# Performance work log

Measured on AMD Instinct MI355X. Metric: run time of the kernel, lower is better.

Reference implementation:

```python
import jax, jax.numpy as jnp
import numpy as np

B, S, D, H, DH = 4, 2048, 512, 8, 64  # batch, seq, input_dim, heads, per-head output_dim


def setup_inputs() -> dict:
    key = jax.random.key(0)
    ks = jax.random.split(key, 10)
    scale = 0.02
    inp = {
        "x": jax.random.normal(ks[0], (B, S, D), dtype=jnp.float32),
        "biological_mask": jnp.ones((B, S), dtype=bool),
        "Wq": jax.random.normal(ks[1], (D, H * DH), dtype=jnp.float32) * scale,
        "bq": jnp.zeros((H * DH,), dtype=jnp.float32),
        "Wk": jax.random.normal(ks[2], (D, H * DH), dtype=jnp.float32) * scale,
        "bk": jnp.zeros((H * DH,), dtype=jnp.float32),
        "Wv": jax.random.normal(ks[3], (D, H * DH), dtype=jnp.float32) * scale,
        "bv": jnp.zeros((H * DH,), dtype=jnp.float32),
        "Wo": jax.random.normal(ks[4], (H * DH, DH), dtype=jnp.float32) * scale,
        "bo": jnp.zeros((DH,), dtype=jnp.float32),
        "prior_weight": jnp.full((1,), 0.1, dtype=jnp.float32),
    }
    return inp


def reference(x, biological_mask, Wq, bq, Wk, bk, Wv, bv, Wo, bo, prior_weight):
    b, s, _ = x.shape
    inv_sqrt_dh = jnp.float32(1.0 / np.sqrt(DH))
    # projections -> [B,H,S,DH]
    q = (x @ Wq + bq).reshape(b, s, H, DH).transpose(0, 2, 1, 3)
    k = (x @ Wk + bk).reshape(b, s, H, DH).transpose(0, 2, 1, 3)
    v = (x @ Wv + bv).reshape(b, s, H, DH).transpose(0, 2, 1, 3)
    # scores [B,H,S,S]
    scores = jnp.einsum("bhqd,bhkd->bhqk", q, k) * inv_sqrt_dh
    # biological prior: identity matrix, broadcast over batch and heads
    prior = jnp.eye(s, dtype=scores.dtype)[None, None, :, :]
    scores = scores + prior_weight[0] * prior
    attn = jax.nn.softmax(scores, axis=-1)  # dropout is identity in eval mode
    attended = jnp.einsum("bhqk,bhkd->bhqd", attn, v)
    attended = attended.transpose(0, 2, 1, 3).reshape(b, s, H * DH)
    return attended @ Wo + bo
```

## Files before the change

### kernel.cpp

```cpp
#include <hip/hip_runtime.h>
#include <hip/hip_bf16.h>

#define B_ 4
#define S_ 2048
#define D_ 512
#define H_ 8
#define DH_ 64
#define HD_ 512
#define M_ 8192
#define QKVN 1536
#define QKN 1024
#define LOG2E 1.4426950408889634f

typedef __attribute__((ext_vector_type(8))) short bf16x8;
typedef __attribute__((ext_vector_type(4))) float f32x4;
typedef unsigned short u16;

__device__ inline u16 f2bf(float f) {
    __hip_bfloat16 h = __float2bfloat16(f);
    return *reinterpret_cast<u16*>(&h);
}

__device__ inline void async_cp16(const void* g, void* l) {
    __builtin_amdgcn_global_load_lds(
        (const __attribute__((address_space(1))) unsigned int*)g,
        (__attribute__((address_space(3))) unsigned int*)l, 16, 0, 0);
}

__global__ __launch_bounds__(256) void castbf(const float* __restrict__ src,
                                              u16* __restrict__ dst, int n8)
{
    int i = blockIdx.x * 256 + threadIdx.x;
    if (i < n8) {
        float4 a = *reinterpret_cast<const float4*>(&src[(size_t)i * 8]);
        float4 b = *reinterpret_cast<const float4*>(&src[(size_t)i * 8 + 4]);
        bf16x8 o;
        o[0] = f2bf(a.x); o[1] = f2bf(a.y); o[2] = f2bf(a.z); o[3] = f2bf(a.w);
        o[4] = f2bf(b.x); o[5] = f2bf(b.y); o[6] = f2bf(b.z); o[7] = f2bf(b.w);
        *reinterpret_cast<bf16x8*>(&dst[(size_t)i * 8]) = o;
    }
}

__global__ __launch_bounds__(256) void wprep(
    const float* __restrict__ Wq, const float* __restrict__ Wk,
    const float* __restrict__ Wv, const float* __restrict__ Wo,
    u16* __restrict__ WqkvT, u16* __restrict__ WoT)
{
    const int z = blockIdx.z;
    const float* src; u16* dst; int R, C;
    if (z < 3) { src = (z == 0) ? Wq : (z == 1) ? Wk : Wv;
                 dst = WqkvT + (size_t)z * 512 * 512; R = 512; C = 512; }
    else       { if (blockIdx.x) return; src = Wo; dst = WoT; R = 512; C = 64; }

    __shared__ u16 T[64][65];
    const int tid = threadIdx.x;
    const int c0 = blockIdx.x * 64, r0 = blockIdx.y * 64;
#pragma unroll
    for (int i = 0; i < 4; ++i) {
        int idx = i * 256 + tid;
        int r = idx >> 4, q4 = (idx & 15) << 2;
        float4 vv = *reinterpret_cast<const float4*>(&src[(size_t)(r0 + r) * C + c0 + q4]);
        T[r][q4 + 0] = f2bf(vv.x); T[r][q4 + 1] = f2bf(vv.y);
        T[r][q4 + 2] = f2bf(vv.z); T[r][q4 + 3] = f2bf(vv.w);
    }
    __syncthreads();
#pragma unroll
    for (int i = 0; i < 2; ++i) {
        int idx = i * 256 + tid;
        int cc = idx >> 3, jj = idx & 7;
        bf16x8 o;
#pragma unroll
        for (int e = 0; e < 8; ++e) o[e] = (short)T[jj * 8 + e][cc];
        *reinterpret_cast<bf16x8*>(&dst[(size_t)(c0 + cc) * R + r0 + jj * 8]) = o;
    }
}

__global__ __launch_bounds__(256) void gemm_qkv(
    const u16* __restrict__ A, const u16* __restrict__ BT,
    const float* __restrict__ bq, const float* __restrict__ bk,
    const float* __restrict__ bv, u16* __restrict__ qk,
    u16* __restrict__ vT, float qscale)
{
    __shared__ __align__(16) u16 As[128 * 64];
    __shared__ __align__(16) u16 Bs[128 * 64];
    const int tid = threadIdx.x, lane = tid & 63, w = tid >> 6;
    const int l15 = lane & 15, l4 = lane >> 4;
    const int tm = blockIdx.y * 128, tn = blockIdx.x * 128;
    const int wm = (w >> 1) * 64, wn = (w & 1) * 64;

    f32x4 acc[4][4] = {};

    for (int k0 = 0; k0 < 512; k0 += 64) {
#pragma unroll
        for (int i = 0; i < 4; ++i) {
            int call = w * 4 + i;
            int c = call * 64 + lane;
            int r = c >> 3, j = c & 7;
            async_cp16(A + (size_t)(tm + r) * 512 + k0 + ((j ^ (r & 7)) << 3),
                       &As[call * 512]);
            async_cp16(BT + (size_t)(tn + r) * 512 + k0 + ((j ^ (r & 7)) << 3),
                       &Bs[call * 512]);
        }
        __syncthreads();
#pragma unroll
        for (int ks = 0; ks < 2; ++ks) {
            bf16x8 af[4], bf[4];
#pragma unroll
            for (int mf = 0; mf < 4; ++mf) {
                int r = wm + mf * 16 + l15;
                int j = ks * 4 + l4;
                af[mf] = *reinterpret_cast<const bf16x8*>(&As[(r * 8 + (j ^ (r & 7))) * 8]);
            }
#pragma unroll
            for (int nf = 0; nf < 4; ++nf) {
                int r = wn + nf * 16 + l15;
                int j = ks * 4 + l4;
                bf[nf] = *reinterpret_cast<const bf16x8*>(&Bs[(r * 8 + (j ^ (r & 7))) * 8]);
            }
#pragma unroll
            for (int mf = 0; mf < 4; ++mf)
#pragma unroll
                for (int nf = 0; nf < 4; ++nf)
                    acc[mf][nf] = __builtin_amdgcn_mfma_f32_16x16x32_bf16(
                        af[mf], bf[nf], acc[mf][nf], 0, 0, 0);
        }
        __syncthreads();
    }
#pragma unroll
    for (int nf = 0; nf < 4; ++nf) {
        const int col = tn + wn + nf * 16 + l15;
        if (col < QKN) {
            const float bias_v = (col < 512) ? bq[col] : bk[col - 512];
            const float scl = (col < 512) ? qscale : 1.0f;
#pragma unroll
            for (int mf = 0; mf < 4; ++mf)
#pragma unroll
                for (int r = 0; r < 4; ++r) {
                    int row = tm + wm + mf * 16 + l4 * 4 + r;
                    qk[(size_t)row * QKN + col] = f2bf((acc[mf][nf][r] + bias_v) * scl);
                }
        } else {
            const int dcol = col - QKN;
            const float bias_v = bv[dcol];
            const int hh = dcol >> 6, dd = dcol & 63;
#pragma unroll
            for (int mf = 0; mf < 4; ++mf) {
                int row0 = tm + wm + mf * 16 + l4 * 4;
                int bb = row0 >> 11, s0 = row0 & 2047;
                ushort4 pk;
                pk.x = f2bf(acc[mf][nf][0] + bias_v);
                pk.y = f2bf(acc[mf][nf][1] + bias_v);
                pk.z = f2bf(acc[mf][nf][2] + bias_v);
                pk.w = f2bf(acc[mf][nf][3] + bias_v);
                *reinterpret_cast<ushort4*>(
                    &vT[((size_t)(bb * 8 + hh) * 64 + dd) * S_ + s0]) = pk;
            }
        }
    }
}

__global__ __launch_bounds__(256) void flash_mfma(
    const u16* __restrict__ qk, const u16* __restrict__ vT,
    const float* __restrict__ pw_ptr, u16* __restrict__ att)
{
    __shared__ __align__(16) u16 Kb[2][4096];
    __shared__ __align__(16) u16 Vb[2][4096];
    __shared__ __align__(16) u16 Ps[4][1024];

    const int tid = threadIdx.x, lane = tid & 63, w = tid >> 6;
    const int l15 = lane & 15, l4 = lane >> 4;
    const int bid = blockIdx.x;
    const int x = bid & 7, g = bid >> 3;
    const int bh = x * 4 + (g >> 5), qt = g & 31;
    const int h = bh & 7, b = bh >> 3;
    const float pwl = pw_ptr[0] * LOG2E;

    const u16* qbase = qk + (size_t)b * S_ * QKN + h * 64;
    const u16* kbase = qbase + 512;
    const u16* vtb   = vT + (size_t)bh * DH_ * S_;

    const int sq = qt * 64 + w * 16 + l15;
    bf16x8 qa0 = *reinterpret_cast<const bf16x8*>(&qbase[(size_t)sq * QKN + l4 * 8]);
    bf16x8 qa1 = *reinterpret_cast<const bf16x8*>(&qbase[(size_t)sq * QKN + 32 + l4 * 8]);

    f32x4 accv[4] = {};
    float l_r[4] = {};

#define STAGE(buf, jj) do {                                                        \
    _Pragma("unroll")                                                              \
    for (int i_ = 0; i_ < 2; ++i_) {                                               \
        int call_ = w * 2 + i_;                                                    \
        int c_ = call_ * 64 + lane;                                                \
        int r_ = c_ >> 3, j_ = c_ & 7;                                             \
        async_cp16(kbase + (size_t)((jj) + r_) * QKN + ((j_ ^ (r_ & 7)) << 3),     \
                   &Kb[buf][call_ * 512]);                                         \
        async_cp16(vtb + (size_t)r_ * S_ + (jj) + ((j_ ^ (r_ & 7)) << 3),          \
                   &Vb[buf][call_ * 512]);                                         \
    } } while (0)

    STAGE(0, 0);
    __syncthreads();
    int cur = 0;

    for (int t = 0; t < 32; ++t) {
        const int j0 = t << 6;
        if (t < 31) STAGE(cur ^ 1, j0 + 64);

        f32x4 s[4] = {};
        __builtin_amdgcn_s_setprio(1);
#pragma unroll
        for (int c = 0; c < 4; ++c)
#pragma unroll
            for (int ks = 0; ks < 2; ++ks) {
                int rr = c * 16 + l15;
                int j = ks * 4 + l4;
                bf16x8 kb = *reinterpret_cast<const bf16x8*>(
                    &Kb[cur][(rr * 8 + (j ^ (rr & 7))) * 8]);
                s[c] = __builtin_amdgcn_mfma_f32_16x16x32_bf16(
                    (ks == 0) ? qa0 : qa1, kb, s[c], 0, 0, 0);
            }
        __builtin_amdgcn_s_setprio(0);

        if (t == qt) {
#pragma unroll
            for (int c = 0; c < 4; ++c) {
                int col_g = j0 + c * 16 + l15;
#pragma unroll
                for (int r = 0; r < 4; ++r)
                    if (qt * 64 + w * 16 + l4 * 4 + r == col_g) s[c][r] += pwl;
            }
        }

#pragma unroll
        for (int c = 0; c < 4; ++c)
#pragma unroll
            for (int r = 0; r < 4; ++r) {
                float p = exp2f(s[c][r]);
                l_r[r] += p;
                int rr = l4 * 4 + r;
                Ps[w][rr * 64 + ((c * 16 + l15) ^ ((rr & 7) << 3))] = f2bf(p);
            }

        bf16x8 pa0 = *reinterpret_cast<const bf16x8*>(
            &Ps[w][l15 * 64 + (((0 * 4 + l4) ^ (l15 & 7)) << 3)]);
        bf16x8 pa1 = *reinterpret_cast<const bf16x8*>(
            &Ps[w][l15 * 64 + (((1 * 4 + l4) ^ (l15 & 7)) << 3)]);

        __builtin_amdgcn_s_setprio(1);
#pragma unroll
        for (int n = 0; n < 4; ++n)
#pragma unroll
            for (int ks = 0; ks < 2; ++ks) {
                int d = n * 16 + l15;
                int j = ks * 4 + l4;
                bf16x8 vb = *reinterpret_cast<const bf16x8*>(
                    &Vb[cur][(d * 8 + (j ^ (d & 7))) * 8]);
                accv[n] = __builtin_amdgcn_mfma_f32_16x16x32_bf16(
                    (ks == 0) ? pa0 : pa1, vb, accv[n], 0, 0, 0);
            }
        __builtin_amdgcn_s_setprio(0);

        __syncthreads();
        cur ^= 1;
    }
#undef STAGE

#pragma unroll
    for (int r = 0; r < 4; ++r) {
        float tsum = l_r[r];
        tsum += __shfl_xor(tsum, 1); tsum += __shfl_xor(tsum, 2);
        tsum += __shfl_xor(tsum, 4); tsum += __shfl_xor(tsum, 8);
        float inv = 1.0f / tsum;
        int row = qt * 64 + w * 16 + l4 * 4 + r;
#pragma unroll
        for (int n = 0; n < 4; ++n)
            att[(size_t)(b * S_ + row) * HD_ + h * 64 + n * 16 + l15] =
                f2bf(accv[n][r] * inv);
    }
}

__global__ __launch_bounds__(64) void out_proj(
    const u16* __restrict__ att, const u16* __restrict__ WoT,
    const float* __restrict__ bo, float* __restrict__ out)
{
    const int lane = threadIdx.x;
    const int l15 = lane & 15, l4 = lane >> 4;
    const int row0 = blockIdx.x * 16;

    f32x4 acc[4] = {};
#pragma unroll 4
    for (int ks = 0; ks < 16; ++ks) {
        bf16x8 a = *reinterpret_cast<const bf16x8*>(
            &att[(size_t)(row0 + l15) * 512 + ks * 32 + l4 * 8]);
#pragma unroll
        for (int nf = 0; nf < 4; ++nf) {
            bf16x8 bb = *reinterpret_cast<const bf16x8*>(
                &WoT[(size_t)(nf * 16 + l15) * 512 + ks * 32 + l4 * 8]);
            acc[nf] = __builtin_amdgcn_mfma_f32_16x16x32_bf16(a, bb, acc[nf], 0, 0, 0);
        }
    }
#pragma unroll
    for (int nf = 0; nf < 4; ++nf) {
        int n = nf * 16 + l15;
        float bias_v = bo[n];
#pragma unroll
        for (int r = 0; r < 4; ++r)
            out[(size_t)(row0 + l4 * 4 + r) * 64 + n] = acc[nf][r] + bias_v;
    }
}

extern "C" void kernel_launch(void* const* d_in, const int* in_sizes, int n_in,
                              void* d_out, int out_size, void* d_ws, size_t ws_size,
                              hipStream_t stream)
{
    const float* x  = (const float*)d_in[0];
    const float* Wq = (const float*)d_in[2];
    const float* bq = (const float*)d_in[3];
    const float* Wk = (const float*)d_in[4];
    const float* bk = (const float*)d_in[5];
    const float* Wv = (const float*)d_in[6];
    const float* bv = (const float*)d_in[7];
    const float* Wo = (const float*)d_in[8];
    const float* bo = (const float*)d_in[9];
    const float* pw = (const float*)d_in[10];

    u16* ws = (u16*)d_ws;
    size_t o = 0;
    u16* xb    = ws + o; o += (size_t)M_ * D_;
    u16* WqkvT = ws + o; o += (size_t)QKVN * D_;
    u16* WoT   = ws + o; o += (size_t)DH_ * HD_;
    u16* qkb   = ws + o; o += (size_t)M_ * QKN;
    u16* vTt   = ws + o; o += (size_t)M_ * HD_;
    u16* att   = ws + o; o += (size_t)M_ * HD_;

    dim3 blk(256);
    castbf<<<dim3(M_ * D_ / 8 / 256), blk, 0, stream>>>(x, xb, M_ * D_ / 8);
    wprep<<<dim3(8, 8, 4), blk, 0, stream>>>(Wq, Wk, Wv, Wo, WqkvT, WoT);

    gemm_qkv<<<dim3(QKVN / 128, M_ / 128), blk, 0, stream>>>(
        xb, WqkvT, bq, bk, bv, qkb, vTt, 0.125f * LOG2E);

    flash_mfma<<<dim3(1024), blk, 0, stream>>>(qkb, vTt, pw, att);

    out_proj<<<dim3(M_ / 16), dim3(64), 0, stream>>>(att, WoT, bo, (float*)d_out);
}
```

Baseline: 120.9 us.

## Double flash query tile per block and load V directly from global

Each block now handles 128 query rows, with each wave covering 32 rows as two 16-row fragments, so every K tile in LDS is reused across twice as many queries. The grid shrinks from 1024 to 512 blocks. The score MMA is transposed (K as A operand, Q as B), P is written to LDS with packed 64-bit stores, and V fragments are read straight from global memory rather than staged through LDS. This cuts LDS traffic and K reloads, but it raises register pressure, halves the number of blocks, and exposes uncached global V load latency inside the loop.

```diff
diff --git a/kernel.cpp b/kernel.cpp
--- a/kernel.cpp
+++ b/kernel.cpp
@@ -15,6 +15,7 @@
 typedef __attribute__((ext_vector_type(8))) short bf16x8;
 typedef __attribute__((ext_vector_type(4))) float f32x4;
 typedef unsigned short u16;
+typedef unsigned int u32;
 
 __device__ inline u16 f2bf(float f) {
     __hip_bfloat16 h = __float2bfloat16(f);
@@ -164,14 +165,13 @@
     const float* __restrict__ pw_ptr, u16* __restrict__ att)
 {
     __shared__ __align__(16) u16 Kb[2][4096];
-    __shared__ __align__(16) u16 Vb[2][4096];
-    __shared__ __align__(16) u16 Ps[4][1024];
+    __shared__ __align__(16) u16 Ps[4][2048];
 
     const int tid = threadIdx.x, lane = tid & 63, w = tid >> 6;
     const int l15 = lane & 15, l4 = lane >> 4;
     const int bid = blockIdx.x;
     const int x = bid & 7, g = bid >> 3;
-    const int bh = x * 4 + (g >> 5), qt = g & 31;
+    const int bh = x * 4 + (g >> 4), qt = g & 15;
     const int h = bh & 7, b = bh >> 3;
     const float pwl = pw_ptr[0] * LOG2E;
 
@@ -179,12 +179,18 @@
     const u16* kbase = qbase + 512;
     const u16* vtb   = vT + (size_t)bh * DH_ * S_;
 
-    const int sq = qt * 64 + w * 16 + l15;
-    bf16x8 qa0 = *reinterpret_cast<const bf16x8*>(&qbase[(size_t)sq * QKN + l4 * 8]);
-    bf16x8 qa1 = *reinterpret_cast<const bf16x8*>(&qbase[(size_t)sq * QKN + 32 + l4 * 8]);
-
-    f32x4 accv[4] = {};
-    float l_r[4] = {};
+    const int qrow0 = qt * 128 + w * 32;
+    bf16x8 qb_[2][2];
+#pragma unroll
+    for (int nf = 0; nf < 2; ++nf)
+#pragma unroll
+        for (int ks = 0; ks < 2; ++ks)
+            qb_[nf][ks] = *reinterpret_cast<const bf16x8*>(
+                &qbase[(size_t)(qrow0 + nf * 16 + l15) * QKN + ks * 32 + l4 * 8]);
+
+    f32x4 accv[2][4] = {};
+    float l_r[2] = {0.f, 0.f};
+    const int diag_t = qrow0 >> 6;
 
 #define STAGE(buf, jj) do {                                                        \
     _Pragma("unroll")                                                              \
@@ -194,69 +200,86 @@
         int r_ = c_ >> 3, j_ = c_ & 7;                                             \
         async_cp16(kbase + (size_t)((jj) + r_) * QKN + ((j_ ^ (r_ & 7)) << 3),     \
                    &Kb[buf][call_ * 512]);                                         \
-        async_cp16(vtb + (size_t)r_ * S_ + (jj) + ((j_ ^ (r_ & 7)) << 3),          \
-                   &Vb[buf][call_ * 512]);                                         \
     } } while (0)
 
     STAGE(0, 0);
     __syncthreads();
     int cur = 0;
 
-    for (int t = 0; t < 32; ++t) {
+    for (int t = 0; t < 16 * 2; ++t) {
         const int j0 = t << 6;
         if (t < 31) STAGE(cur ^ 1, j0 + 64);
 
-        f32x4 s[4] = {};
+        bf16x8 vb_[4][2];
+#pragma unroll
+        for (int nf = 0; nf < 4; ++nf)
+#pragma unroll
+            for (int ks = 0; ks < 2; ++ks)
+                vb_[nf][ks] = *reinterpret_cast<const bf16x8*>(
+                    &vtb[(size_t)(nf * 16 + l15) * S_ + j0 + ks * 32 + l4 * 8]);
+
+        f32x4 s[4][2] = {};
         __builtin_amdgcn_s_setprio(1);
 #pragma unroll
         for (int c = 0; c < 4; ++c)
 #pragma unroll
             for (int ks = 0; ks < 2; ++ks) {
                 int rr = c * 16 + l15;
-                int j = ks * 4 + l4;
-                bf16x8 kb = *reinterpret_cast<const bf16x8*>(
-                    &Kb[cur][(rr * 8 + (j ^ (rr & 7))) * 8]);
-                s[c] = __builtin_amdgcn_mfma_f32_16x16x32_bf16(
-                    (ks == 0) ? qa0 : qa1, kb, s[c], 0, 0, 0);
+                int jj2 = ks * 4 + l4;
+                bf16x8 ka = *reinterpret_cast<const bf16x8*>(
+                    &Kb[cur][(rr * 8 + (jj2 ^ (rr & 7))) * 8]);
+                s[c][0] = __builtin_amdgcn_mfma_f32_16x16x32_bf16(ka, qb_[0][ks], s[c][0], 0, 0, 0);
+                s[c][1] = __builtin_amdgcn_mfma_f32_16x16x32_bf16(ka, qb_[1][ks], s[c][1], 0, 0, 0);
             }
         __builtin_amdgcn_s_setprio(0);
 
-        if (t == qt) {
+        if (t == diag_t) {
+#pragma unroll
+            for (int c = 0; c < 4; ++c)
+#pragma unroll
+                for (int nf = 0; nf < 2; ++nf)
+#pragma unroll
+                    for (int r = 0; r < 4; ++r)
+                        if (j0 + c * 16 + l4 * 4 + r == qrow0 + nf * 16 + l15)
+                            s[c][nf][r] += pwl;
+        }
+
+#pragma unroll
+        for (int nf = 0; nf < 2; ++nf) {
+            const int prow = nf * 16 + l15;
+            const int pswz = (prow & 7) << 3;
 #pragma unroll
             for (int c = 0; c < 4; ++c) {
-                int col_g = j0 + c * 16 + l15;
-#pragma unroll
-                for (int r = 0; r < 4; ++r)
-                    if (qt * 64 + w * 16 + l4 * 4 + r == col_g) s[c][r] += pwl;
-            }
-        }
-
-#pragma unroll
-        for (int c = 0; c < 4; ++c)
-#pragma unroll
-            for (int r = 0; r < 4; ++r) {
-                float p = exp2f(s[c][r]);
-                l_r[r] += p;
-                int rr = l4 * 4 + r;
-                Ps[w][rr * 64 + ((c * 16 + l15) ^ ((rr & 7) << 3))] = f2bf(p);
-            }
-
-        bf16x8 pa0 = *reinterpret_cast<const bf16x8*>(
-            &Ps[w][l15 * 64 + (((0 * 4 + l4) ^ (l15 & 7)) << 3)]);
-        bf16x8 pa1 = *reinterpret_cast<const bf16x8*>(
-            &Ps[w][l15 * 64 + (((1 * 4 + l4) ^ (l15 & 7)) << 3)]);
+                float p0 = exp2f(s[c][nf][0]);
+                float p1 = exp2f(s[c][nf][1]);
+                float p2 = exp2f(s[c][nf][2]);
+                float p3 = exp2f(s[c][nf][3]);
+                l_r[nf] += (p0 + p1) + (p2 + p3);
+                uint2 pk;
+                pk.x = (u32)f2bf(p0) | ((u32)f2bf(p1) << 16);
+                pk.y = (u32)f2bf(p2) | ((u32)f2bf(p3) << 16);
+                *reinterpret_cast<uint2*>(
+                    &Ps[w][prow * 64 + ((c * 16 + l4 * 4) ^ pswz)]) = pk;
+            }
+        }
+
+        bf16x8 pa[2][2];
+#pragma unroll
+        for (int mf = 0; mf < 2; ++mf)
+#pragma unroll
+            for (int ks = 0; ks < 2; ++ks) {
+                int prow = mf * 16 + l15;
+                pa[mf][ks] = *reinterpret_cast<const bf16x8*>(
+                    &Ps[w][prow * 64 + ((ks * 32 + l4 * 8) ^ ((prow & 7) << 3))]);
+            }
 
         __builtin_amdgcn_s_setprio(1);
 #pragma unroll
-        for (int n = 0; n < 4; ++n)
+        for (int nf = 0; nf < 4; ++nf)
 #pragma unroll
             for (int ks = 0; ks < 2; ++ks) {
-                int d = n * 16 + l15;
-                int j = ks * 4 + l4;
-                bf16x8 vb = *reinterpret_cast<const bf16x8*>(
-                    &Vb[cur][(d * 8 + (j ^ (d & 7))) * 8]);
-                accv[n] = __builtin_amdgcn_mfma_f32_16x16x32_bf16(
-                    (ks == 0) ? pa0 : pa1, vb, accv[n], 0, 0, 0);
+                accv[0][nf] = __builtin_amdgcn_mfma_f32_16x16x32_bf16(pa[0][ks], vb_[nf][ks], accv[0][nf], 0, 0, 0);
+                accv[1][nf] = __builtin_amdgcn_mfma_f32_16x16x32_bf16(pa[1][ks], vb_[nf][ks], accv[1][nf], 0, 0, 0);
             }
         __builtin_amdgcn_s_setprio(0);
 
@@ -265,18 +288,25 @@
     }
 #undef STAGE
 
-#pragma unroll
-    for (int r = 0; r < 4; ++r) {
-        float tsum = l_r[r];
-        tsum += __shfl_xor(tsum, 1); tsum += __shfl_xor(tsum, 2);
-        tsum += __shfl_xor(tsum, 4); tsum += __shfl_xor(tsum, 8);
-        float inv = 1.0f / tsum;
-        int row = qt * 64 + w * 16 + l4 * 4 + r;
-#pragma unroll
-        for (int n = 0; n < 4; ++n)
-            att[(size_t)(b * S_ + row) * HD_ + h * 64 + n * 16 + l15] =
-                f2bf(accv[n][r] * inv);
-    }
+    float lt[2];
+#pragma unroll
+    for (int nf = 0; nf < 2; ++nf) {
+        float t2 = l_r[nf];
+        t2 += __shfl_xor(t2, 16);
+        t2 += __shfl_xor(t2, 32);
+        lt[nf] = t2;
+    }
+#pragma unroll
+    for (int mf = 0; mf < 2; ++mf)
+#pragma unroll
+        for (int r = 0; r < 4; ++r) {
+            float inv = 1.0f / __shfl(lt[mf], l4 * 4 + r);
+            int row = qrow0 + mf * 16 + l4 * 4 + r;
+#pragma unroll
+            for (int nf = 0; nf < 4; ++nf)
+                att[(size_t)(b * S_ + row) * HD_ + h * 64 + nf * 16 + l15] =
+                    f2bf(accv[mf][nf][r] * inv);
+        }
 }
 
 __global__ __launch_bounds__(64) void out_proj(
@@ -340,7 +370,7 @@
     gemm_qkv<<<dim3(QKVN / 128, M_ / 128), blk, 0, stream>>>(
         xb, WqkvT, bq, bk, bv, qkb, vTt, 0.125f * LOG2E);
 
-    flash_mfma<<<dim3(1024), blk, 0, stream>>>(qkb, vTt, pw, att);
+    flash_mfma<<<dim3(512), blk, 0, stream>>>(qkb, vTt, pw, att);
 
     out_proj<<<dim3(M_ / 16), dim3(64), 0, stream>>>(att, WoT, bo, (float*)d_out);
 }
```

Measured after the change: 129.4 us. 1.07x slower.

## Compute transposed QK^T in registers to feed PV MFMA without LDS round-trip

Applied to the files above, without the earlier changes.

Swaps MFMA operand order so the score tile comes out transposed (keys along the register dimension), and permutes K rows at staging time so each lane's score registers directly form the bf16x8 A-operand for the PV MFMA. This removes the per-wave Ps LDS buffer, its stores/loads, and the associated bank traffic. The row sum now reduces across lanes via xor 16/32 and is fetched with a shuffle at the end. Launch bounds add a min-blocks hint of 4, which may constrain registers.

```diff
diff --git a/kernel.cpp b/kernel.cpp
--- a/kernel.cpp
+++ b/kernel.cpp
@@ -159,13 +159,12 @@
     }
 }
 
-__global__ __launch_bounds__(256) void flash_mfma(
+__global__ __launch_bounds__(256, 4) void flash_mfma(
     const u16* __restrict__ qk, const u16* __restrict__ vT,
     const float* __restrict__ pw_ptr, u16* __restrict__ att)
 {
     __shared__ __align__(16) u16 Kb[2][4096];
     __shared__ __align__(16) u16 Vb[2][4096];
-    __shared__ __align__(16) u16 Ps[4][1024];
 
     const int tid = threadIdx.x, lane = tid & 63, w = tid >> 6;
     const int l15 = lane & 15, l4 = lane >> 4;
@@ -179,22 +178,28 @@
     const u16* kbase = qbase + 512;
     const u16* vtb   = vT + (size_t)bh * DH_ * S_;
 
-    const int sq = qt * 64 + w * 16 + l15;
-    bf16x8 qa0 = *reinterpret_cast<const bf16x8*>(&qbase[(size_t)sq * QKN + l4 * 8]);
-    bf16x8 qa1 = *reinterpret_cast<const bf16x8*>(&qbase[(size_t)sq * QKN + 32 + l4 * 8]);
+    const int qrow0 = qt * 64 + w * 16;
+    bf16x8 qb[2];
+#pragma unroll
+    for (int ks2 = 0; ks2 < 2; ++ks2)
+        qb[ks2] = *reinterpret_cast<const bf16x8*>(
+            &qbase[(size_t)(qrow0 + l15) * QKN + ks2 * 32 + l4 * 8]);
 
     f32x4 accv[4] = {};
-    float l_r[4] = {};
+    float l_r = 0.f;
+    const int diag_t = qt;
 
 #define STAGE(buf, jj) do {                                                        \
     _Pragma("unroll")                                                              \
     for (int i_ = 0; i_ < 2; ++i_) {                                               \
         int call_ = w * 2 + i_;                                                    \
         int c_ = call_ * 64 + lane;                                                \
-        int r_ = c_ >> 3, j_ = c_ & 7;                                             \
-        async_cp16(kbase + (size_t)((jj) + r_) * QKN + ((j_ ^ (r_ & 7)) << 3),     \
+        int rho_ = c_ >> 3, j_ = c_ & 7;                                           \
+        int pi_ = (rho_ & 32) | ((rho_ & 12) << 1) | ((rho_ & 16) >> 2)            \
+                | (rho_ & 3);                                                      \
+        async_cp16(kbase + (size_t)((jj) + pi_) * QKN + ((j_ ^ (rho_ & 7)) << 3),  \
                    &Kb[buf][call_ * 512]);                                         \
-        async_cp16(vtb + (size_t)r_ * S_ + (jj) + ((j_ ^ (r_ & 7)) << 3),          \
+        async_cp16(vtb + (size_t)rho_ * S_ + (jj) + ((j_ ^ (rho_ & 7)) << 3),      \
                    &Vb[buf][call_ * 512]);                                         \
     } } while (0)
 
@@ -211,53 +216,49 @@
 #pragma unroll
         for (int c = 0; c < 4; ++c)
 #pragma unroll
+            for (int ks2 = 0; ks2 < 2; ++ks2) {
+                const int rr = c * 16 + l15;
+                const int sl = ks2 * 4 + l4;
+                bf16x8 ka = *reinterpret_cast<const bf16x8*>(
+                    &Kb[cur][(rr * 8 + (sl ^ (rr & 7))) * 8]);
+                s[c] = __builtin_amdgcn_mfma_f32_16x16x32_bf16(ka, qb[ks2], s[c], 0, 0, 0);
+            }
+        __builtin_amdgcn_s_setprio(0);
+
+        if (t == diag_t) {
+#pragma unroll
+            for (int c = 0; c < 4; ++c)
+#pragma unroll
+                for (int r = 0; r < 4; ++r) {
+                    int kv = (c >> 1) * 32 + l4 * 8 + (c & 1) * 4 + r;
+                    if (j0 + kv == qrow0 + l15) s[c][r] += pwl;
+                }
+        }
+
+        bf16x8 pa[2];
+#pragma unroll
+        for (int ks = 0; ks < 2; ++ks)
+#pragma unroll
+            for (int d2 = 0; d2 < 2; ++d2)
+#pragma unroll
+                for (int r = 0; r < 4; ++r) {
+                    float p = exp2f(s[ks * 2 + d2][r]);
+                    l_r += p;
+                    pa[ks][d2 * 4 + r] = (short)f2bf(p);
+                }
+
+        __builtin_amdgcn_s_setprio(1);
+#pragma unroll
+        for (int nf = 0; nf < 4; ++nf) {
+            const int d = nf * 16 + l15;
+#pragma unroll
             for (int ks = 0; ks < 2; ++ks) {
-                int rr = c * 16 + l15;
-                int j = ks * 4 + l4;
-                bf16x8 kb = *reinterpret_cast<const bf16x8*>(
-                    &Kb[cur][(rr * 8 + (j ^ (rr & 7))) * 8]);
-                s[c] = __builtin_amdgcn_mfma_f32_16x16x32_bf16(
-                    (ks == 0) ? qa0 : qa1, kb, s[c], 0, 0, 0);
-            }
-        __builtin_amdgcn_s_setprio(0);
-
-        if (t == qt) {
-#pragma unroll
-            for (int c = 0; c < 4; ++c) {
-                int col_g = j0 + c * 16 + l15;
-#pragma unroll
-                for (int r = 0; r < 4; ++r)
-                    if (qt * 64 + w * 16 + l4 * 4 + r == col_g) s[c][r] += pwl;
-            }
-        }
-
-#pragma unroll
-        for (int c = 0; c < 4; ++c)
-#pragma unroll
-            for (int r = 0; r < 4; ++r) {
-                float p = exp2f(s[c][r]);
-                l_r[r] += p;
-                int rr = l4 * 4 + r;
-                Ps[w][rr * 64 + ((c * 16 + l15) ^ ((rr & 7) << 3))] = f2bf(p);
-            }
-
-        bf16x8 pa0 = *reinterpret_cast<const bf16x8*>(
-            &Ps[w][l15 * 64 + (((0 * 4 + l4) ^ (l15 & 7)) << 3)]);
-        bf16x8 pa1 = *reinterpret_cast<const bf16x8*>(
-            &Ps[w][l15 * 64 + (((1 * 4 + l4) ^ (l15 & 7)) << 3)]);
-
-        __builtin_amdgcn_s_setprio(1);
-#pragma unroll
-        for (int n = 0; n < 4; ++n)
-#pragma unroll
-            for (int ks = 0; ks < 2; ++ks) {
-                int d = n * 16 + l15;
-                int j = ks * 4 + l4;
+                const int sl = ks * 4 + l4;
                 bf16x8 vb = *reinterpret_cast<const bf16x8*>(
-                    &Vb[cur][(d * 8 + (j ^ (d & 7))) * 8]);
-                accv[n] = __builtin_amdgcn_mfma_f32_16x16x32_bf16(
-                    (ks == 0) ? pa0 : pa1, vb, accv[n], 0, 0, 0);
-            }
+                    &Vb[cur][(d * 8 + (sl ^ (d & 7))) * 8]);
+                accv[nf] = __builtin_amdgcn_mfma_f32_16x16x32_bf16(pa[ks], vb, accv[nf], 0, 0, 0);
+            }
+        }
         __builtin_amdgcn_s_setprio(0);
 
         __syncthreads();
@@ -265,17 +266,17 @@
     }
 #undef STAGE
 
+    float lt = l_r;
+    lt += __shfl_xor(lt, 16);
+    lt += __shfl_xor(lt, 32);
 #pragma unroll
     for (int r = 0; r < 4; ++r) {
-        float tsum = l_r[r];
-        tsum += __shfl_xor(tsum, 1); tsum += __shfl_xor(tsum, 2);
-        tsum += __shfl_xor(tsum, 4); tsum += __shfl_xor(tsum, 8);
-        float inv = 1.0f / tsum;
-        int row = qt * 64 + w * 16 + l4 * 4 + r;
-#pragma unroll
-        for (int n = 0; n < 4; ++n)
-            att[(size_t)(b * S_ + row) * HD_ + h * 64 + n * 16 + l15] =
-                f2bf(accv[n][r] * inv);
+        float inv = 1.0f / __shfl(lt, l4 * 4 + r);
+        int row = qrow0 + l4 * 4 + r;
+#pragma unroll
+        for (int nf = 0; nf < 4; ++nf)
+            att[(size_t)(b * S_ + row) * HD_ + h * 64 + nf * 16 + l15] =
+                f2bf(accv[nf][r] * inv);
     }
 }
 
```

Measured after the change: 107.9 us. 1.12x faster.
